# Optimization experiments

Hardware: AMD Instinct MI355X
Metric: run time of the kernel (lower is better)

## Reference

```python
import jax, jax.numpy as jnp
import numpy as np

N_NODES = 50000
N_HOPS = 4
N_EDGES = 800000
NFEAT = 512
HIDDEN = 512
NCLASS = 128
ATT_HID = 64


def setup_inputs() -> dict:
    key = jax.random.key(0)
    ks = jax.random.split(key, 12)
    s = lambda *sh: 1.0 / np.sqrt(sh[0])
    inp = {}
    inp['x'] = jax.random.normal(ks[0], (N_NODES, NFEAT), dtype=jnp.float32)
    inp['W1'] = jax.random.normal(ks[1], (NFEAT, HIDDEN), dtype=jnp.float32) * s(NFEAT)
    inp['W2'] = jax.random.normal(ks[2], (HIDDEN, NCLASS), dtype=jnp.float32) * s(HIDDEN)
    inp['b2'] = jax.random.normal(ks[3], (NCLASS,), dtype=jnp.float32) * 0.01
    inp['Wg'] = jax.random.normal(ks[4], (NCLASS, NCLASS), dtype=jnp.float32) * s(NCLASS)
    inp['Wa'] = jax.random.normal(ks[5], (2 * NCLASS, ATT_HID), dtype=jnp.float32) * s(2 * NCLASS)
    inp['ba'] = jax.random.normal(ks[6], (ATT_HID,), dtype=jnp.float32) * 0.01
    inp['va'] = jax.random.normal(ks[7], (ATT_HID,), dtype=jnp.float32) * s(ATT_HID)
    inp['adj_values'] = jax.random.uniform(ks[8], (N_HOPS, N_EDGES), dtype=jnp.float32)
    inp['adj_indices'] = jax.random.randint(ks[9], (N_HOPS, 2, N_EDGES), 0, N_NODES, dtype=jnp.int32)
    inp['idx'] = jnp.arange(N_NODES, dtype=jnp.int32)
    return inp


def reference(x, W1, W2, b2, Wg, Wa, ba, va, adj_values, adj_indices, idx):
    # x: [N, nfeat] -> relu(linear1) -> linear2 : [N, C]
    z = jax.nn.relu(x @ W1) @ W2 + b2  # [N, C]
    anchor = z[idx]                    # [Na, C]
    na = idx.shape[0]
    n_hops = adj_indices.shape[0]
    embs = [anchor]
    for h in range(n_hops):  # fixed small structural loop over hops
        rows = adj_indices[h, 0]  # destination anchor row per edge
        cols = adj_indices[h, 1]  # source node per edge
        # sparse matmul: agg[r] = sum_e v_e * z[cols_e]  (LayerConvol)
        agg = jax.ops.segment_sum(adj_values[h][:, None] * z[cols], rows, num_segments=na)
        embs.append(agg @ Wg)  # [Na, C]
    seq = jnp.stack(embs, axis=1)  # [Na, H+1, C]
    # AttenMlp: additive attention of anchor query over hop embeddings
    q = jnp.broadcast_to(anchor[:, None, :], seq.shape)       # [Na, H+1, C]
    feat = jnp.concatenate([q, seq], axis=-1)                 # [Na, H+1, 2C]
    scores = jnp.tanh(feat @ Wa + ba) @ va                    # [Na, H+1]
    alpha = jax.nn.softmax(scores, axis=1)
    out = jnp.einsum('nh,nhc->nc', alpha, seq)                # [Na, C]
    return jax.nn.log_softmax(out, axis=1)
```

## Files before the change

### kernel.cpp

```cpp
#include <hip/hip_runtime.h>

#define NA    50000
#define NFEAT 512
#define HID   512
#define NC    128
#define AH    64
#define NE    800000
#define NHOP  4
#define NBUCK 196
#define CAPB  5120

typedef __bf16 bf16x8 __attribute__((ext_vector_type(8)));
typedef float  f32x4  __attribute__((ext_vector_type(4)));

__device__ __forceinline__ unsigned short f2bf(float f){
  union { float f; unsigned u; } a; a.f = f;
  return (unsigned short)((a.u + 0x7fffu + ((a.u >> 16) & 1u)) >> 16);
}
__device__ __forceinline__ float bf2f(unsigned short h){
  union { unsigned u; float f; } a; a.u = ((unsigned)h) << 16;
  return a.f;
}
__device__ __forceinline__ float uasf(unsigned u){
  union { unsigned u; float f; } a; a.u = u;
  return a.f;
}
__device__ __forceinline__ float tanh_fast(float x){
  x = fminf(15.f, fmaxf(-15.f, x));
  float e = __expf(2.f * x);
  return (e - 1.f) / (e + 1.f);
}

__device__ __forceinline__ void g2l16(const void* g, void* l){
  __builtin_amdgcn_global_load_lds(
      (const __attribute__((address_space(1))) void*)g,
      (__attribute__((address_space(3))) void*)l, 16, 0, 0);
}


__global__ void cast_x_kernel(const float* __restrict__ in, unsigned short* __restrict__ out, int n4){
  int i = blockIdx.x * 256 + threadIdx.x;
  if (i >= n4) return;
  float4 v = reinterpret_cast<const float4*>(in)[i];
  ushort4 o; o.x = f2bf(v.x); o.y = f2bf(v.y); o.z = f2bf(v.z); o.w = f2bf(v.w);
  reinterpret_cast<ushort4*>(out)[i] = o;
}

__global__ void transpose_cast_kernel(const float* __restrict__ in, unsigned short* __restrict__ out,
                                      int R, int N){
  int i = blockIdx.x * 256 + threadIdx.x;
  if (i >= R * N) return;
  int n = i / R, k = i - n * R;
  out[i] = f2bf(in[(size_t)k * N + n]);
}

__global__ void build_wa_kernel(const float* __restrict__ Wa, unsigned short* __restrict__ WaT){
  int i = blockIdx.x * 256 + threadIdx.x;
  if (i >= 128 * 128) return;
  int n = i >> 7, k = i & 127;
  float v = (n < 64) ? Wa[(size_t)k * AH + n] : Wa[(size_t)(128 + k) * AH + (n - 64)];
  WaT[i] = f2bf(v);
}

__global__ void wfuse_kernel(const float* __restrict__ Wa, const float* __restrict__ Wg,
                             unsigned short* __restrict__ WfuseT){
  int i = blockIdx.x * 256 + threadIdx.x;
  if (i >= 64 * 128) return;
  int j = i >> 7, n = i & 127;
  float s = 0.f;
  for (int k = 0; k < 128; k++)
    s += Wa[(size_t)(128 + k) * AH + j] * Wg[(size_t)n * 128 + k];
  WfuseT[i] = f2bf(s);
}

template<int OP, int SWZ>
__global__ __launch_bounds__(256) void gemm_bt(
    const unsigned short* __restrict__ A, const unsigned short* __restrict__ BT,
    float* __restrict__ Cf, unsigned short* __restrict__ Cb,
    const float* __restrict__ bias,
    int M, int N, int K)
{
  int row0, col0;
  if (SWZ){
    const int xcd = blockIdx.x & 7, slot = blockIdx.x >> 3;
    const int r = xcd * 49 + (slot >> 2);
    if (r >= 391) return;
    row0 = r * 128; col0 = (slot & 3) * 128;
  } else {
    row0 = blockIdx.x * 128; col0 = blockIdx.y * 128;
  }
  __shared__ unsigned short As[128 * 32];
  __shared__ unsigned short Bs[128 * 32];
  const int tid = threadIdx.x;
  const int wave = tid >> 6, lane = tid & 63;
  const int wr = (wave >> 1) * 64, wc = (wave & 1) * 64;
  f32x4 acc[4][4];
  #pragma unroll
  for (int m = 0; m < 4; m++)
    #pragma unroll
    for (int n = 0; n < 4; n++) acc[m][n] = (f32x4){0.f, 0.f, 0.f, 0.f};
  const int lrow = lane >> 2, lk = (lane & 3) * 8;

  for (int k0 = 0; k0 < K; k0 += 32){
    __syncthreads();
    #pragma unroll
    for (int j = 0; j < 2; j++){
      const int rb = (wave * 2 + j) * 16;
      const int ra = rb + lrow;
      int gr = row0 + ra; gr = gr < M ? gr : M - 1;
      g2l16(A + (size_t)gr * K + k0 + lk, As + rb * 32);
      int gc = col0 + ra; gc = gc < N ? gc : N - 1;
      g2l16(BT + (size_t)gc * K + k0 + lk, Bs + rb * 32);
    }
    __syncthreads();
    bf16x8 af[4], bfr[4];
    #pragma unroll
    for (int m = 0; m < 4; m++)
      af[m] = *reinterpret_cast<const bf16x8*>(&As[(wr + m * 16 + (lane & 15)) * 32 + (lane >> 4) * 8]);
    #pragma unroll
    for (int n = 0; n < 4; n++)
      bfr[n] = *reinterpret_cast<const bf16x8*>(&Bs[(wc + n * 16 + (lane & 15)) * 32 + (lane >> 4) * 8]);
    #pragma unroll
    for (int m = 0; m < 4; m++)
      #pragma unroll
      for (int n = 0; n < 4; n++)
        acc[m][n] = __builtin_amdgcn_mfma_f32_16x16x32_bf16(af[m], bfr[n], acc[m][n], 0, 0, 0);
  }

  const int rbase = row0 + wr + (lane >> 4) * 4;
  const int cbase = col0 + wc + (lane & 15);
  #pragma unroll
  for (int m = 0; m < 4; m++){
    #pragma unroll
    for (int n = 0; n < 4; n++){
      const int col = cbase + n * 16;
      #pragma unroll
      for (int i = 0; i < 4; i++){
        const int row = rbase + m * 16 + i;
        if (row < M && col < N){
          float v = acc[m][n][i];
          if (OP == 0){ v = v > 0.f ? v : 0.f; Cb[(size_t)row * N + col] = f2bf(v); }
          else {
            v += bias[col];
            Cf[(size_t)row * N + col] = v;
            Cb[(size_t)row * N + col] = f2bf(v);
          }
        }
      }
    }
  }
}

__global__ __launch_bounds__(256) void gemm_sweep(
    const unsigned short* __restrict__ aggbf, const unsigned short* __restrict__ zbf,
    const unsigned short* __restrict__ WgT, const unsigned short* __restrict__ WfuseT,
    const unsigned short* __restrict__ WaT,
    unsigned short* __restrict__ embs, unsigned short* __restrict__ EW, float* __restrict__ ZW)
{
  const int zi = blockIdx.z;
  const unsigned short* A; const unsigned short* BT;
  unsigned short* Cb = nullptr; float* Cf = nullptr; int N;
  if (zi < 4)      { A = aggbf + (size_t)zi * NA * NC;       BT = WgT;    Cb = embs + (size_t)zi * NA * NC; N = 128; }
  else if (zi < 8) { A = aggbf + (size_t)(zi - 4) * NA * NC; BT = WfuseT; Cb = EW + (size_t)(zi - 4) * NA * AH; N = 64; }
  else             { A = zbf;                                BT = WaT;    Cf = ZW; N = 128; }

  __shared__ unsigned short As[128 * 32];
  __shared__ unsigned short Bs[128 * 32];
  const int tid = threadIdx.x;
  const int wave = tid >> 6, lane = tid & 63;
  const int row0 = blockIdx.x * 128;
  const int wr = (wave >> 1) * 64, wc = (wave & 1) * 64;
  f32x4 acc[4][4];
  #pragma unroll
  for (int m = 0; m < 4; m++)
    #pragma unroll
    for (int n = 0; n < 4; n++) acc[m][n] = (f32x4){0.f, 0.f, 0.f, 0.f};

  for (int k0 = 0; k0 < 128; k0 += 32){
    __syncthreads();
    #pragma unroll
    for (int j = 0; j < 2; j++){
      const int rb = (wave * 2 + j) * 16;
      int gr = row0 + rb + (lane >> 2); gr = gr < NA ? gr : NA - 1;
      g2l16(A + (size_t)gr * 128 + k0 + (lane & 3) * 8, As + rb * 32);
      int gc = rb + (lane >> 2); gc = gc < N ? gc : N - 1;
      g2l16(BT + (size_t)gc * 128 + k0 + (lane & 3) * 8, Bs + rb * 32);
    }
    __syncthreads();
    bf16x8 bfr[4];
    #pragma unroll
    for (int n = 0; n < 4; n++)
      bfr[n] = *reinterpret_cast<const bf16x8*>(&Bs[(wc + n * 16 + (lane & 15)) * 32 + (lane >> 4) * 8]);
    #pragma unroll
    for (int m = 0; m < 4; m++){
      bf16x8 a = *reinterpret_cast<const bf16x8*>(&As[(wr + m * 16 + (lane & 15)) * 32 + (lane >> 4) * 8]);
      #pragma unroll
      for (int n = 0; n < 4; n++)
        acc[m][n] = __builtin_amdgcn_mfma_f32_16x16x32_bf16(a, bfr[n], acc[m][n], 0, 0, 0);
    }
  }

  const int rbase = row0 + wr + (lane >> 4) * 4;
  const int cbase = wc + (lane & 15);
  #pragma unroll
  for (int m = 0; m < 4; m++){
    #pragma unroll
    for (int n = 0; n < 4; n++){
      const int col = cbase + n * 16;
      #pragma unroll
      for (int i = 0; i < 4; i++){
        const int row = rbase + m * 16 + i;
        if (row < NA && col < N){
          float v = acc[m][n][i];
          if (Cf) Cf[(size_t)row * N + col] = v;
          else    Cb[(size_t)row * N + col] = f2bf(v);
        }
      }
    }
  }
}

__global__ __launch_bounds__(256) void binA_kernel(
    const int* __restrict__ adji, const float* __restrict__ adjv,
    int* __restrict__ fill, long long* __restrict__ binned)
{
  const int h = blockIdx.y, tid = threadIdx.x;
  const int e0 = blockIdx.x * 2048;
  __shared__ int lhist[NBUCK], lbase[NBUCK], lfill[NBUCK];
  for (int i = tid; i < NBUCK; i += 256){ lhist[i] = 0; lfill[i] = 0; }
  __syncthreads();
  int rr[8]; unsigned hh[8]; float vv[8];
  #pragma unroll
  for (int k = 0; k < 8; k++){
    int e = e0 + k * 256 + tid;
    bool ok = e < NE;
    int r = ok ? adji[(size_t)h * 2 * NE + e] : -1;
    int c = ok ? adji[(size_t)h * 2 * NE + NE + e] : 0;
    vv[k] = ok ? adjv[(size_t)h * NE + e] : 0.f;
    rr[k] = r;
    hh[k] = ((unsigned)(r & 255) << 17) | (unsigned)c;
    if (ok) atomicAdd(&lhist[r >> 8], 1);
  }
  __syncthreads();
  if (tid < NBUCK) lbase[tid] = atomicAdd(&fill[h * NBUCK + tid], lhist[tid]);
  __syncthreads();
  #pragma unroll
  for (int k = 0; k < 8; k++){
    if (rr[k] >= 0){
      int b = rr[k] >> 8;
      int p = lbase[b] + atomicAdd(&lfill[b], 1);
      if (p < CAPB)
        binned[((size_t)(h * NBUCK + b)) * CAPB + p] =
            ((long long)hh[k] << 32) | (unsigned)__float_as_int(vv[k]);
    }
  }
}

__global__ __launch_bounds__(1024) void bscan_kernel(const int* __restrict__ fill,
                                                     int* __restrict__ bbase, int* __restrict__ offs){
  __shared__ int tmp[1024];
  int tid = threadIdx.x;
  int v = (tid < NHOP * NBUCK) ? fill[tid] : 0;
  tmp[tid] = v; __syncthreads();
  for (int o = 1; o < 1024; o <<= 1){
    int t = (tid >= o) ? tmp[tid - o] : 0;
    __syncthreads();
    tmp[tid] += t;
    __syncthreads();
  }
  if (tid < NHOP * NBUCK) bbase[tid] = tmp[tid] - v;
  if (tid == 0) offs[NHOP * NA] = NHOP * NE;
}

__global__ __launch_bounds__(256) void binB_kernel(
    const int* __restrict__ fill, const int* __restrict__ bbase,
    const long long* __restrict__ binned,
    int* __restrict__ offs, long long* __restrict__ pvc)
{
  const int b = blockIdx.x, h = blockIdx.y, tid = threadIdx.x;
  const int hb = h * NBUCK + b;
  const int cnt = min(fill[hb], CAPB);
  const long long* src = binned + (size_t)hb * CAPB;
  const int gbase = bbase[hb];
  const int rowbase = b << 8;
  const int nrows = min(256, NA - rowbase);
  __shared__ long long sdata[CAPB];
  __shared__ int lhist[256], lpre[256], lfill2[256];
  lhist[tid] = 0; lfill2[tid] = 0;
  __syncthreads();
  for (int p = tid; p < cnt; p += 256)
    atomicAdd(&lhist[(unsigned)(src[p] >> 32) >> 17], 1);
  __syncthreads();
  int v = lhist[tid]; lpre[tid] = v; __syncthreads();
  for (int o = 1; o < 256; o <<= 1){
    int t = (tid >= o) ? lpre[tid - o] : 0;
    __syncthreads();
    lpre[tid] += t;
    __syncthreads();
  }
  int excl = lpre[tid] - v;
  if (tid < nrows) offs[h * NA + rowbase + tid] = gbase + excl;
  lpre[tid] = excl;
  __syncthreads();
  for (int p = tid; p < cnt; p += 256){
    long long rec = src[p];
    unsigned hi = (unsigned)(rec >> 32);
    int lr = hi >> 17;
    long long out = (rec & 0xffffffffLL) | ((long long)(hi & 0x1ffffu) << 32);
    int pos = lpre[lr] + atomicAdd(&lfill2[lr], 1);
    if (pos < CAPB) sdata[pos] = out;
    else            pvc[(size_t)gbase + pos] = out;
  }
  __syncthreads();
  for (int p = tid; p < cnt; p += 256)
    pvc[(size_t)gbase + p] = sdata[p];
}

#define GR 4
__global__ __launch_bounds__(256) void gather_kernel(
    const int* __restrict__ offs, const long long* __restrict__ pvc,
    const unsigned short* __restrict__ zbf, unsigned short* __restrict__ aggbf)
{
  const int h = blockIdx.y;
  const int w = threadIdx.x >> 6, lane = threadIdx.x & 63;
  const int row = blockIdx.x * GR + w;
  const int base = h * NA + row;
  const int s = offs[base], e = offs[base + 1];
  __shared__ alignas(16) long long srec[GR][64];
  const unsigned* z32 = (const unsigned*)zbf;
  const int4* sr2 = (const int4*)&srec[w][0];
  float a0 = 0.f, a1 = 0.f, b0 = 0.f, b1 = 0.f;
  for (int p0 = s; p0 < e; p0 += 64){
    long long r = 0;
    if (p0 + lane < e) r = __builtin_nontemporal_load(&pvc[p0 + lane]);
    srec[w][lane] = r;
    const int quads = (min(64, e - p0) + 3) >> 2;
    #pragma unroll 2
    for (int q = 0; q < quads; q++){
      int4 ra = sr2[2 * q], rb = sr2[2 * q + 1];
      unsigned z0 = z32[((unsigned)ra.y << 6) + lane];
      unsigned z1 = z32[((unsigned)ra.w << 6) + lane];
      unsigned z2 = z32[((unsigned)rb.y << 6) + lane];
      unsigned z3 = z32[((unsigned)rb.w << 6) + lane];
      float v0 = uasf((unsigned)ra.x), v1 = uasf((unsigned)ra.z);
      float v2 = uasf((unsigned)rb.x), v3 = uasf((unsigned)rb.z);
      a0 += v0 * uasf(z0 << 16); a1 += v0 * uasf(z0 & 0xffff0000u);
      b0 += v1 * uasf(z1 << 16); b1 += v1 * uasf(z1 & 0xffff0000u);
      a0 += v2 * uasf(z2 << 16); a1 += v2 * uasf(z2 & 0xffff0000u);
      b0 += v3 * uasf(z3 << 16); b1 += v3 * uasf(z3 & 0xffff0000u);
    }
  }
  ushort2 o; o.x = f2bf(a0 + b0); o.y = f2bf(a1 + b1);
  *reinterpret_cast<ushort2*>(aggbf + (size_t)base * NC + lane * 2) = o;
}

__global__ __launch_bounds__(256) void final_kernel(
    const float* __restrict__ z, const unsigned short* __restrict__ embs,
    const float* __restrict__ ZW, const unsigned short* __restrict__ EW,
    const float* __restrict__ ba, const float* __restrict__ va,
    const int* __restrict__ idx, float* __restrict__ out)
{
  int tid = threadIdx.x, wave = tid >> 6, lane = tid & 63;
  int n = blockIdx.x * 4 + wave;
  if (n >= NA) return;
  int an = idx[n];
  float qa = ZW[(size_t)an * NC + lane] + ba[lane];
  float vaj = va[lane];
  float sc[5];
  {
    float s0 = ZW[(size_t)an * NC + 64 + lane];
    float t = tanh_fast(qa + s0) * vaj;
    #pragma unroll
    for (int o = 32; o; o >>= 1) t += __shfl_xor(t, o);
    sc[0] = t;
  }
  #pragma unroll
  for (int h = 1; h < 5; h++){
    float sh = bf2f(EW[((size_t)(h - 1) * NA + n) * AH + lane]);
    float t = tanh_fast(qa + sh) * vaj;
    #pragma unroll
    for (int o = 32; o; o >>= 1) t += __shfl_xor(t, o);
    sc[h] = t;
  }
  float m = sc[0];
  #pragma unroll
  for (int h = 1; h < 5; h++) m = fmaxf(m, sc[h]);
  float al[5], den = 0.f;
  #pragma unroll
  for (int h = 0; h < 5; h++){ al[h] = __expf(sc[h] - m); den += al[h]; }
  float inv = 1.f / den;
  float o0 = al[0] * z[(size_t)an * NC + lane];
  float o1 = al[0] * z[(size_t)an * NC + 64 + lane];
  #pragma unroll
  for (int h = 1; h < 5; h++){
    o0 += al[h] * bf2f(embs[((size_t)(h - 1) * NA + n) * NC + lane]);
    o1 += al[h] * bf2f(embs[((size_t)(h - 1) * NA + n) * NC + 64 + lane]);
  }
  o0 *= inv; o1 *= inv;
  float mx = fmaxf(o0, o1);
  #pragma unroll
  for (int o = 32; o; o >>= 1) mx = fmaxf(mx, __shfl_xor(mx, o));
  float se = __expf(o0 - mx) + __expf(o1 - mx);
  #pragma unroll
  for (int o = 32; o; o >>= 1) se += __shfl_xor(se, o);
  float ls = __logf(se);
  out[(size_t)n * NC + lane]      = o0 - mx - ls;
  out[(size_t)n * NC + 64 + lane] = o1 - mx - ls;
}


extern "C" void kernel_launch(void* const* d_in, const int* in_sizes, int n_in,
                              void* d_out, int out_size, void* d_ws, size_t ws_size,
                              hipStream_t stream)
{
  const float* x    = (const float*)d_in[0];
  const float* W1   = (const float*)d_in[1];
  const float* W2   = (const float*)d_in[2];
  const float* b2   = (const float*)d_in[3];
  const float* Wg   = (const float*)d_in[4];
  const float* Wa   = (const float*)d_in[5];
  const float* ba   = (const float*)d_in[6];
  const float* va   = (const float*)d_in[7];
  const float* adjv = (const float*)d_in[8];
  const int*   adji = (const int*)d_in[9];
  const int*   idx  = (const int*)d_in[10];
  float* out = (float*)d_out;
  (void)in_sizes; (void)n_in; (void)out_size; (void)ws_size;

  char* w = (char*)d_ws;
  auto alloc = [&](size_t b) -> char* { char* p = w; w += (b + 255) & ~(size_t)255; return p; };
  unsigned short* Scr1 = (unsigned short*)alloc((size_t)NA * NFEAT * 2);
  unsigned short* Hbuf = (unsigned short*)alloc((size_t)NA * HID * 2);
  unsigned short* W1T  = (unsigned short*)alloc((size_t)HID * NFEAT * 2);
  unsigned short* W2T  = (unsigned short*)alloc((size_t)NC * HID * 2);
  unsigned short* WgT  = (unsigned short*)alloc((size_t)NC * NC * 2);
  unsigned short* WaT  = (unsigned short*)alloc((size_t)NC * NC * 2);
  unsigned short* WfuseT = (unsigned short*)alloc((size_t)AH * NC * 2);
  float*          z    = (float*)alloc((size_t)NA * NC * 4);
  unsigned short* zbf  = (unsigned short*)alloc((size_t)NA * NC * 2);
  float*          ZW   = (float*)alloc((size_t)NA * NC * 4);
  int* fill  = (int*)alloc((size_t)NHOP * NBUCK * 4);
  int* bbase = (int*)alloc((size_t)NHOP * NBUCK * 4);
  int* offs  = (int*)alloc(((size_t)NHOP * NA + 1) * 4);
  long long* pvc = (long long*)alloc((size_t)NHOP * NE * 8);
  unsigned short* Xbf   = Scr1;
  long long* binned     = (long long*)Scr1;
  unsigned short* embs  = Scr1;
  unsigned short* aggbf = Hbuf;
  unsigned short* EW    = (unsigned short*)pvc;

  cast_x_kernel<<<dim3((NA * NFEAT / 4 + 255) / 256), 256, 0, stream>>>(x, Xbf, NA * NFEAT / 4);
  transpose_cast_kernel<<<dim3((NFEAT * HID + 255) / 256), 256, 0, stream>>>(W1, W1T, NFEAT, HID);
  transpose_cast_kernel<<<dim3((HID * NC + 255) / 256), 256, 0, stream>>>(W2, W2T, HID, NC);
  transpose_cast_kernel<<<dim3((NC * NC + 255) / 256), 256, 0, stream>>>(Wg, WgT, NC, NC);
  build_wa_kernel<<<dim3(64), 256, 0, stream>>>(Wa, WaT);
  wfuse_kernel<<<dim3(32), 256, 0, stream>>>(Wa, Wg, WfuseT);

  gemm_bt<0, 1><<<dim3(1568, 1, 1), 256, 0, stream>>>(Xbf, W1T, nullptr, Hbuf, nullptr, NA, HID, NFEAT);
  gemm_bt<1, 0><<<dim3(391, 1, 1), 256, 0, stream>>>(Hbuf, W2T, z, zbf, b2, NA, NC, HID);

  hipMemsetAsync(fill, 0, (size_t)NHOP * NBUCK * 4, stream);
  binA_kernel<<<dim3((NE + 2047) / 2048, NHOP), 256, 0, stream>>>(adji, adjv, fill, binned);
  bscan_kernel<<<dim3(1), 1024, 0, stream>>>(fill, bbase, offs);
  binB_kernel<<<dim3(NBUCK, NHOP), 256, 0, stream>>>(fill, bbase, binned, offs, pvc);

  gather_kernel<<<dim3(NA / GR, NHOP), 256, 0, stream>>>(offs, pvc, zbf, aggbf);
  gemm_sweep<<<dim3(391, 1, 9), 256, 0, stream>>>(aggbf, zbf, WgT, WfuseT, WaT, embs, EW, ZW);

  final_kernel<<<dim3(NA / 4), 256, 0, stream>>>(z, embs, ZW, EW, ba, va, idx, out);
}
```

Baseline: 353.0 us.

## Gather from column-tiled z copy so each block covers one 32-column slice

The second GEMM now also writes z in a tiled layout (4 slices of 32 columns, each node-major), and the gather kernel is split so each block handles one 32-column slice for 4 rows. Each wave processes 4 edges at once with 16 lanes per edge, then reduces across lane groups with shuffles. The aim is a smaller working set per block (a 3.2MB slice rather than the whole z) for better L2 hit rates on random gathers. In exchange, edge records are read 4 times, there are 4x as many blocks, the GEMM does an extra scattered store, and there is a shuffle reduction.

```diff
diff --git a/kernel.cpp b/kernel.cpp
--- a/kernel.cpp
+++ b/kernel.cpp
@@ -77,6 +77,7 @@
 __global__ __launch_bounds__(256) void gemm_bt(
     const unsigned short* __restrict__ A, const unsigned short* __restrict__ BT,
     float* __restrict__ Cf, unsigned short* __restrict__ Cb,
+    unsigned short* __restrict__ Czt,
     const float* __restrict__ bias,
     int M, int N, int K)
 {
@@ -143,7 +144,9 @@
           else {
             v += bias[col];
             Cf[(size_t)row * N + col] = v;
-            Cb[(size_t)row * N + col] = f2bf(v);
+            unsigned short b = f2bf(v);
+            Cb[(size_t)row * N + col] = b;
+            Czt[((size_t)(col >> 5) * NA + row) * 32 + (col & 31)] = b;
           }
         }
       }
@@ -319,39 +322,41 @@
 #define GR 4
 __global__ __launch_bounds__(256) void gather_kernel(
     const int* __restrict__ offs, const long long* __restrict__ pvc,
-    const unsigned short* __restrict__ zbf, unsigned short* __restrict__ aggbf)
-{
+    const unsigned short* __restrict__ zt, unsigned short* __restrict__ aggbf)
+{
+  const int t  = (blockIdx.x & 7) >> 1;
+  const int rc = (blockIdx.x >> 3) * 2 + (blockIdx.x & 1);
   const int h = blockIdx.y;
   const int w = threadIdx.x >> 6, lane = threadIdx.x & 63;
-  const int row = blockIdx.x * GR + w;
+  const int g = lane >> 4, cl = lane & 15;
+  const int row = rc * GR + w;
   const int base = h * NA + row;
   const int s = offs[base], e = offs[base + 1];
   __shared__ alignas(16) long long srec[GR][64];
-  const unsigned* z32 = (const unsigned*)zbf;
-  const int4* sr2 = (const int4*)&srec[w][0];
-  float a0 = 0.f, a1 = 0.f, b0 = 0.f, b1 = 0.f;
+  const unsigned* zt32 = (const unsigned*)(zt + (size_t)t * NA * 32);
+  const long long* sr = &srec[w][0];
+  float a0 = 0.f, a1 = 0.f;
   for (int p0 = s; p0 < e; p0 += 64){
     long long r = 0;
     if (p0 + lane < e) r = __builtin_nontemporal_load(&pvc[p0 + lane]);
     srec[w][lane] = r;
     const int quads = (min(64, e - p0) + 3) >> 2;
-    #pragma unroll 2
+    #pragma unroll 4
     for (int q = 0; q < quads; q++){
-      int4 ra = sr2[2 * q], rb = sr2[2 * q + 1];
-      unsigned z0 = z32[((unsigned)ra.y << 6) + lane];
-      unsigned z1 = z32[((unsigned)ra.w << 6) + lane];
-      unsigned z2 = z32[((unsigned)rb.y << 6) + lane];
-      unsigned z3 = z32[((unsigned)rb.w << 6) + lane];
-      float v0 = uasf((unsigned)ra.x), v1 = uasf((unsigned)ra.z);
-      float v2 = uasf((unsigned)rb.x), v3 = uasf((unsigned)rb.z);
-      a0 += v0 * uasf(z0 << 16); a1 += v0 * uasf(z0 & 0xffff0000u);
-      b0 += v1 * uasf(z1 << 16); b1 += v1 * uasf(z1 & 0xffff0000u);
-      a0 += v2 * uasf(z2 << 16); a1 += v2 * uasf(z2 & 0xffff0000u);
-      b0 += v3 * uasf(z3 << 16); b1 += v3 * uasf(z3 & 0xffff0000u);
-    }
-  }
-  ushort2 o; o.x = f2bf(a0 + b0); o.y = f2bf(a1 + b1);
-  *reinterpret_cast<ushort2*>(aggbf + (size_t)base * NC + lane * 2) = o;
+      long long rec = sr[q * 4 + g];
+      float    v = uasf((unsigned)rec);
+      unsigned c = (unsigned)(rec >> 32);
+      unsigned zd = zt32[(c << 4) + cl];
+      a0 += v * uasf(zd << 16);
+      a1 += v * uasf(zd & 0xffff0000u);
+    }
+  }
+  a0 += __shfl_xor(a0, 16); a0 += __shfl_xor(a0, 32);
+  a1 += __shfl_xor(a1, 16); a1 += __shfl_xor(a1, 32);
+  if (g == 0){
+    ushort2 o; o.x = f2bf(a0); o.y = f2bf(a1);
+    *reinterpret_cast<ushort2*>(aggbf + (size_t)base * NC + t * 32 + cl * 2) = o;
+  }
 }
 
 __global__ __launch_bounds__(256) void final_kernel(
@@ -438,6 +443,7 @@
   unsigned short* WfuseT = (unsigned short*)alloc((size_t)AH * NC * 2);
   float*          z    = (float*)alloc((size_t)NA * NC * 4);
   unsigned short* zbf  = (unsigned short*)alloc((size_t)NA * NC * 2);
+  unsigned short* zt   = (unsigned short*)alloc((size_t)NA * NC * 2);
   float*          ZW   = (float*)alloc((size_t)NA * NC * 4);
   int* fill  = (int*)alloc((size_t)NHOP * NBUCK * 4);
   int* bbase = (int*)alloc((size_t)NHOP * NBUCK * 4);
@@ -456,15 +462,15 @@
   build_wa_kernel<<<dim3(64), 256, 0, stream>>>(Wa, WaT);
   wfuse_kernel<<<dim3(32), 256, 0, stream>>>(Wa, Wg, WfuseT);
 
-  gemm_bt<0, 1><<<dim3(1568, 1, 1), 256, 0, stream>>>(Xbf, W1T, nullptr, Hbuf, nullptr, NA, HID, NFEAT);
-  gemm_bt<1, 0><<<dim3(391, 1, 1), 256, 0, stream>>>(Hbuf, W2T, z, zbf, b2, NA, NC, HID);
+  gemm_bt<0, 1><<<dim3(1568, 1, 1), 256, 0, stream>>>(Xbf, W1T, nullptr, Hbuf, nullptr, nullptr, NA, HID, NFEAT);
+  gemm_bt<1, 0><<<dim3(391, 1, 1), 256, 0, stream>>>(Hbuf, W2T, z, zbf, zt, b2, NA, NC, HID);
 
   hipMemsetAsync(fill, 0, (size_t)NHOP * NBUCK * 4, stream);
   binA_kernel<<<dim3((NE + 2047) / 2048, NHOP), 256, 0, stream>>>(adji, adjv, fill, binned);
   bscan_kernel<<<dim3(1), 1024, 0, stream>>>(fill, bbase, offs);
   binB_kernel<<<dim3(NBUCK, NHOP), 256, 0, stream>>>(fill, bbase, binned, offs, pvc);
 
-  gather_kernel<<<dim3(NA / GR, NHOP), 256, 0, stream>>>(offs, pvc, zbf, aggbf);
+  gather_kernel<<<dim3(50000, NHOP), 256, 0, stream>>>(offs, pvc, zt, aggbf);
   gemm_sweep<<<dim3(391, 1, 9), 256, 0, stream>>>(aggbf, zbf, WgT, WfuseT, WaT, embs, EW, ZW);
 
   final_kernel<<<dim3(NA / 4), 256, 0, stream>>>(z, embs, ZW, EW, ba, va, idx, out);
```

New measurement: 515.2 us. 1.46x slower.
